# Kernel tuning notes

Hardware: AMD Instinct MI355X
Metric: run time of the kernel (lower is better)

## Reference

```python
import jax, jax.numpy as jnp
import numpy as np

EMBED = 128
HEADS = 4
WS = (7, 7)
N = WS[0] * WS[1]  # 49 patches per window
B_ = 8192          # batch * num_windows_total
NW = 64            # windows per image (for mask reshape)


def _rel_pos_index():
    # Deterministic relative-position index table, computed exactly as in build().
    coords = np.stack(np.meshgrid(np.arange(WS[0]), np.arange(WS[1]), indexing='ij'))
    coords = coords.reshape(2, -1)                     # [2, N]
    rel = coords[:, :, None] - coords[:, None, :]      # [2, N, N]
    rel = rel.transpose(1, 2, 0).astype(np.int64)      # [N, N, 2]
    rel[:, :, 0] += WS[0] - 1
    rel[:, :, 1] += WS[1] - 1
    rel[:, :, 0] *= 2 * WS[1] - 1
    return jnp.asarray(rel.sum(-1))                    # [N, N]

REL_IDX = _rel_pos_index()


def setup_inputs() -> dict:
    key = jax.random.key(0)
    ks = jax.random.split(key, 7)
    return {
        'x': jax.random.normal(ks[0], (B_, N, EMBED), jnp.float32),
        'mask': jax.random.normal(ks[1], (NW, N, N), jnp.float32),
        'qkv_w': jax.random.normal(ks[2], (EMBED, 3 * EMBED), jnp.float32) * 0.02,
        'qkv_b': jax.random.normal(ks[3], (3 * EMBED,), jnp.float32) * 0.02,
        'proj_w': jax.random.normal(ks[4], (EMBED, EMBED), jnp.float32) * 0.02,
        'proj_b': jax.random.normal(ks[5], (EMBED,), jnp.float32) * 0.02,
        'rel_pos_table': jax.random.normal(ks[6], ((2 * WS[0] - 1) * (2 * WS[1] - 1), HEADS), jnp.float32) * 0.02,
    }


def reference(x, mask, qkv_w, qkv_b, proj_w, proj_b, rel_pos_table):
    B, n, C = x.shape
    hd = C // HEADS
    scale = hd ** -0.5
    # qkv projection then faithful row-major reshape [B,N,3C] -> [3,B,H,N,hd]
    qkv = x @ qkv_w + qkv_b                          # [B, N, 3C]
    qkv = qkv.reshape(3, B, HEADS, n, hd)
    q, k, v = qkv[0] * scale, qkv[1], qkv[2]
    attn = jnp.einsum('bhqd,bhkd->bhqk', q, k)       # [B, H, N, N]
    # gathered relative position bias: [N*N, H] -> [H, N, N]
    bias = rel_pos_table[REL_IDX.reshape(-1)].reshape(n, n, HEADS)
    attn = attn + jnp.transpose(bias, (2, 0, 1))[None]
    # additive window mask: reshape to [B/NW, NW, H, N, N]
    attn = attn.reshape(-1, NW, HEADS, n, n) + mask[None, :, None]
    attn = attn.reshape(-1, HEADS, n, n)
    attn = jax.nn.softmax(attn, axis=-1)
    out = jnp.einsum('bhqk,bhkd->bhqd', attn, v)     # [B, H, N, hd]
    out = jnp.transpose(out, (0, 2, 1, 3)).reshape(B, n, C)
    return out @ proj_w + proj_b
```

## Files before the change

### kernel.cpp

```cpp
#include <hip/hip_runtime.h>

typedef __attribute__((ext_vector_type(8))) short short8;
typedef __attribute__((ext_vector_type(4))) float f32x4;

#define Q3 51380224
#define NROWS 401408

#define XB_OFF 0
#define XB_ST 136
#define Q_OFF 8704
#define QK_H 2560
#define QK_ST 40
#define K_OFF 18944
#define VT_OFF 29184
#define VT_H 2304
#define VT_ST 72
#define P_OFF 8704
#define P_ST 72
#define AOUT_OFF 0
#define LDS_EL 38400

#define WQ_EL 0
#define PW_EL 49152
#define T_BYTE 131072

__device__ __forceinline__ unsigned short f2bf(float f) {
    unsigned int u = __float_as_uint(f);
    u += 0x7FFFu + ((u >> 16) & 1u);
    return (unsigned short)(u >> 16);
}

__global__ __launch_bounds__(256) void prep_weights(
    const float* __restrict__ qkv_w, const float* __restrict__ proj_w,
    unsigned short* __restrict__ wq, unsigned short* __restrict__ pw)
{
    int t = blockIdx.x * 256 + threadIdx.x;
    if (t < 49152) {
        int c = t >> 7, k = t & 127;
        wq[t] = f2bf(qkv_w[k * 384 + c]);
    }
    int t2 = t - 49152;
    if (t2 >= 0 && t2 < 16384) {
        int c = t2 >> 7, k = t2 & 127;
        pw[t2] = f2bf(proj_w[k * 128 + c]);
    }
}

__global__ __launch_bounds__(256) void prep_table(
    const float* __restrict__ mask, const float* __restrict__ rpt,
    float* __restrict__ T)
{
    int t = blockIdx.x * 256 + threadIdx.x;
    if (t >= 64 * 4 * 64 * 64) return;
    int j = t & 63, i = (t >> 6) & 63, h = (t >> 12) & 3, w = t >> 14;
    float v;
    if (j >= 49) v = -1e30f;
    else if (i >= 49) v = 0.f;
    else {
        int ri = i / 7, ci = i - ri * 7, rj = j / 7, cj = j - rj * 7;
        int idx = (ri - rj + 6) * 13 + (ci - cj + 6);
        v = (rpt[idx * 4 + h] + mask[(w * 49 + i) * 49 + j]) * 1.4426950408889634f;
    }
    T[t] = v;
}

__global__ __launch_bounds__(512, 4) void winattn(
    const float* __restrict__ x,
    const unsigned short* __restrict__ wq, const unsigned short* __restrict__ pw,
    const float* __restrict__ T,
    const float* __restrict__ qkv_b, const float* __restrict__ proj_b,
    float* __restrict__ out)
{
    __shared__ unsigned short lds[LDS_EL];
    unsigned int* ldsw = (unsigned int*)lds;
    const int b = blockIdx.x;
    const int tid = threadIdx.x;
    const int wid = tid >> 6;
    const int lane = tid & 63;
    const int l15 = lane & 15;
    const int lq = lane >> 4;
    const f32x4 zero = {0.f, 0.f, 0.f, 0.f};
    const float qscale = 0.17677669529663687f * 1.4426950408889634f;

    const int base0 = b * 6272;
    const int r0_0 = base0 / 384,      off_0 = base0 - r0_0 * 384;
    const int base1 = Q3 + base0;
    const int r0_1 = base1 / 384,      off_1 = base1 - r0_1 * 384;
    const int base2 = 2 * Q3 + base0;
    const int r0_2 = base2 / 384,      off_2 = base2 - r0_2 * 384;

    for (int t = tid; t < 4608; t += 512) ldsw[VT_OFF / 2 + t] = 0u;
    for (int t = tid; t < 2400; t += 512) {
        int run = t / 300, rem = t - run * 300;
        int h = run & 3, reg = run >> 2;
        ldsw[(Q_OFF + reg * 10240 + h * QK_H + 49 * QK_ST) / 2 + rem] = 0u;
    }

    for (int t = tid; t < 51 * 32; t += 512) {
        int row = t >> 5, kq = (t & 31) * 4;
        int run = row >= 34 ? 2 : (row >= 17 ? 1 : 0);
        int r0s = run == 2 ? r0_2 : (run == 1 ? r0_1 : r0_0);
        int gr = r0s + row - run * 17;
        float4 v = *(const float4*)&x[gr * 128 + kq];
        uint2 d;
        d.x = (unsigned int)f2bf(v.x) | ((unsigned int)f2bf(v.y) << 16);
        d.y = (unsigned int)f2bf(v.z) | ((unsigned int)f2bf(v.w) << 16);
        *(uint2*)&ldsw[(row * XB_ST + kq) / 2] = d;
    }
    __syncthreads();

    for (int ntj = 0; ntj < 3; ++ntj) {
        const int nt = wid + ntj * 8;
        const int C = nt * 16 + l15;
        short8 bf[4];
        const short8* wrow = (const short8*)&wq[C * 128];
#pragma unroll
        for (int ks = 0; ks < 4; ++ks) bf[ks] = wrow[ks * 4 + lq];
        const float biasv = qkv_b[C];
#pragma unroll
        for (int mt = 0; mt < 4; ++mt) {
            f32x4 acc = zero;
#pragma unroll
            for (int ks = 0; ks < 4; ++ks) {
                short8 a = *(const short8*)&lds[(mt * 16 + l15) * XB_ST + ks * 32 + lq * 8];
                acc = __builtin_amdgcn_mfma_f32_16x16x32_bf16(a, bf[ks], acc, 0, 0, 0);
            }
#pragma unroll
            for (int r = 0; r < 4; ++r) {
                int R = mt * 16 + lq * 4 + r;
                int run = R >= 34 ? 2 : (R >= 17 ? 1 : 0);
                int offs = run == 2 ? off_2 : (run == 1 ? off_1 : off_0);
                int t2 = (R - run * 17) * 384 + C - offs;
                if (t2 >= 0 && t2 < 6272) {
                    int h = t2 / 1568;
                    int rem = t2 - h * 1568;
                    int n = rem >> 5, d = rem & 31;
                    float o = acc[r] + biasv;
                    if (run == 0) o *= qscale;
                    unsigned short val = f2bf(o);
                    if (run == 2) lds[VT_OFF + h * VT_H + d * VT_ST + n] = val;
                    else lds[(run == 1 ? K_OFF : Q_OFF) + h * QK_H + n * QK_ST + d] = val;
                }
            }
        }
    }
    __syncthreads();

    const int h = wid >> 1;
    {
        const int ihalf = wid & 1;
        short8 kf[4];
#pragma unroll
        for (int jt = 0; jt < 4; ++jt)
            kf[jt] = *(const short8*)&lds[K_OFF + h * QK_H + (jt * 16 + l15) * QK_ST + lq * 8];
        f32x4 acc[2][4];
#pragma unroll
        for (int it = 0; it < 2; ++it) {
            short8 qf = *(const short8*)&lds[Q_OFF + h * QK_H + (ihalf * 32 + it * 16 + l15) * QK_ST + lq * 8];
#pragma unroll
            for (int jt = 0; jt < 4; ++jt)
                acc[it][jt] = __builtin_amdgcn_mfma_f32_16x16x32_bf16(qf, kf[jt], zero, 0, 0, 0);
        }
        __syncthreads();
        const float* Tb = T + (((b & 63) * 4 + h) << 12);
#pragma unroll
        for (int it = 0; it < 2; ++it)
#pragma unroll
        for (int r = 0; r < 4; ++r) {
            int i = ihalf * 32 + it * 16 + lq * 4 + r;
            const float* Trow = Tb + i * 64 + l15;
            float s0 = acc[it][0][r] + Trow[0];
            float s1 = acc[it][1][r] + Trow[16];
            float s2 = acc[it][2][r] + Trow[32];
            float s3 = acc[it][3][r] + Trow[48];
            float m = fmaxf(fmaxf(s0, s1), fmaxf(s2, s3));
            m = fmaxf(m, __shfl_xor(m, 1));
            m = fmaxf(m, __shfl_xor(m, 2));
            m = fmaxf(m, __shfl_xor(m, 4));
            m = fmaxf(m, __shfl_xor(m, 8));
            float e0 = exp2f(s0 - m), e1 = exp2f(s1 - m);
            float e2 = exp2f(s2 - m), e3 = exp2f(s3 - m);
            float sum = e0 + e1 + e2 + e3;
            sum += __shfl_xor(sum, 1);
            sum += __shfl_xor(sum, 2);
            sum += __shfl_xor(sum, 4);
            sum += __shfl_xor(sum, 8);
            float inv = 1.f / sum;
            int pb = P_OFF + (h * 64 + i) * P_ST + l15;
            lds[pb +  0] = f2bf(e0 * inv);
            lds[pb + 16] = f2bf(e1 * inv);
            lds[pb + 32] = f2bf(e2 * inv);
            lds[pb + 48] = f2bf(e3 * inv);
        }
    }
    __syncthreads();

    {
        const int dt = wid & 1;
        const int vbase = VT_OFF + h * VT_H + (dt * 16 + l15) * VT_ST + lq * 8;
        short8 vf0 = *(const short8*)&lds[vbase];
        short8 vf1 = *(const short8*)&lds[vbase + 32];
#pragma unroll
        for (int mt = 0; mt < 4; ++mt) {
            int pbase = P_OFF + (h * 64 + mt * 16 + l15) * P_ST + lq * 8;
            short8 a0 = *(const short8*)&lds[pbase];
            short8 a1 = *(const short8*)&lds[pbase + 32];
            f32x4 acc = __builtin_amdgcn_mfma_f32_16x16x32_bf16(a0, vf0, zero, 0, 0, 0);
            acc = __builtin_amdgcn_mfma_f32_16x16x32_bf16(a1, vf1, acc, 0, 0, 0);
#pragma unroll
            for (int r = 0; r < 4; ++r) {
                int i = mt * 16 + lq * 4 + r;
                if (i < 49)
                    lds[AOUT_OFF + i * XB_ST + h * 32 + dt * 16 + l15] = f2bf(acc[r]);
            }
        }
    }
    const int Cp = wid * 16 + l15;
    short8 pf[4];
#pragma unroll
    for (int ks = 0; ks < 4; ++ks)
        pf[ks] = *(const short8*)&pw[Cp * 128 + ks * 32 + lq * 8];
    const float pbv = proj_b[Cp];
    __syncthreads();

#pragma unroll
    for (int mt = 0; mt < 4; ++mt) {
        f32x4 acc = zero;
#pragma unroll
        for (int ks = 0; ks < 4; ++ks) {
            short8 a = *(const short8*)&lds[AOUT_OFF + (mt * 16 + l15) * XB_ST + ks * 32 + lq * 8];
            acc = __builtin_amdgcn_mfma_f32_16x16x32_bf16(a, pf[ks], acc, 0, 0, 0);
        }
#pragma unroll
        for (int r = 0; r < 4; ++r) {
            int R = mt * 16 + lq * 4 + r;
            if (R < 49)
                out[(b * 49 + R) * 128 + Cp] = acc[r] + pbv;
        }
    }
}

extern "C" void kernel_launch(void* const* d_in, const int* in_sizes, int n_in,
                              void* d_out, int out_size, void* d_ws, size_t ws_size,
                              hipStream_t stream) {
    const float* x      = (const float*)d_in[0];
    const float* mask   = (const float*)d_in[1];
    const float* qkv_w  = (const float*)d_in[2];
    const float* qkv_b  = (const float*)d_in[3];
    const float* proj_w = (const float*)d_in[4];
    const float* proj_b = (const float*)d_in[5];
    const float* rpt    = (const float*)d_in[6];
    float* out = (float*)d_out;

    unsigned short* wq = (unsigned short*)d_ws;
    unsigned short* pw = wq + PW_EL - PW_EL + 49152;
    float* T = (float*)((char*)d_ws + T_BYTE);

    prep_weights<<<256, 256, 0, stream>>>(qkv_w, proj_w, wq, pw);
    prep_table<<<4096, 256, 0, stream>>>(mask, rpt, T);
    winattn<<<8192, 512, 0, stream>>>(x, wq, pw, T, qkv_b, proj_b, out);
}
```

Baseline: 307.2 us.

## Precompute QKV scatter-address table and merge prep kernels into one launch

The per-element index arithmetic for scattering QKV results into LDS (division, run selection, bounds checks) is replaced by a precomputed table of LDS addresses. The table is indexed by b%3, since the scatter pattern repeats every three windows, and invalid entries point to a trash slot. The q scale is folded into the x rows converted for the Q run and into the bias, and the two prep kernels are merged into one launch. The aim is to cut integer ALU work and divergence in the QKV epilogue. The cost is an extra global table load per tile and a small added LDS pad.

```diff
diff --git a/kernel.cpp b/kernel.cpp
--- a/kernel.cpp
+++ b/kernel.cpp
@@ -4,7 +4,6 @@
 typedef __attribute__((ext_vector_type(4))) float f32x4;
 
 #define Q3 51380224
-#define NROWS 401408
 
 #define XB_OFF 0
 #define XB_ST 136
@@ -15,14 +14,11 @@
 #define VT_OFF 29184
 #define VT_H 2304
 #define VT_ST 72
+#define TRASH 38400
+#define LDS_EL 38408
 #define P_OFF 8704
 #define P_ST 72
 #define AOUT_OFF 0
-#define LDS_EL 38400
-
-#define WQ_EL 0
-#define PW_EL 49152
-#define T_BYTE 131072
 
 __device__ __forceinline__ unsigned short f2bf(float f) {
     unsigned int u = __float_as_uint(f);
@@ -30,44 +26,65 @@
     return (unsigned short)(u >> 16);
 }
 
-__global__ __launch_bounds__(256) void prep_weights(
+__global__ __launch_bounds__(256) void prep(
     const float* __restrict__ qkv_w, const float* __restrict__ proj_w,
-    unsigned short* __restrict__ wq, unsigned short* __restrict__ pw)
+    const float* __restrict__ mask, const float* __restrict__ rpt,
+    unsigned short* __restrict__ wq, unsigned short* __restrict__ pw,
+    unsigned short* __restrict__ stab, float* __restrict__ T)
 {
     int t = blockIdx.x * 256 + threadIdx.x;
     if (t < 49152) {
         int c = t >> 7, k = t & 127;
         wq[t] = f2bf(qkv_w[k * 384 + c]);
-    }
-    int t2 = t - 49152;
-    if (t2 >= 0 && t2 < 16384) {
-        int c = t2 >> 7, k = t2 & 127;
-        pw[t2] = f2bf(proj_w[k * 128 + c]);
-    }
-}
-
-__global__ __launch_bounds__(256) void prep_table(
-    const float* __restrict__ mask, const float* __restrict__ rpt,
-    float* __restrict__ T)
-{
-    int t = blockIdx.x * 256 + threadIdx.x;
-    if (t >= 64 * 4 * 64 * 64) return;
-    int j = t & 63, i = (t >> 6) & 63, h = (t >> 12) & 3, w = t >> 14;
-    float v;
-    if (j >= 49) v = -1e30f;
-    else if (i >= 49) v = 0.f;
-    else {
-        int ri = i / 7, ci = i - ri * 7, rj = j / 7, cj = j - rj * 7;
-        int idx = (ri - rj + 6) * 13 + (ci - cj + 6);
-        v = (rpt[idx * 4 + h] + mask[(w * 49 + i) * 49 + j]) * 1.4426950408889634f;
-    }
-    T[t] = v;
+        return;
+    }
+    t -= 49152;
+    if (t < 16384) {
+        int c = t >> 7, k = t & 127;
+        pw[t] = f2bf(proj_w[k * 128 + c]);
+        return;
+    }
+    t -= 16384;
+    if (t < 73728) {
+        int R = t & 63;
+        int b3 = t / (384 * 64);
+        int C = (t - b3 * 384 * 64) >> 6;
+        unsigned short el = TRASH;
+        if (R <= 50) {
+            int run = R >= 34 ? 2 : (R >= 17 ? 1 : 0);
+            int sh = run == 0 ? b3 : (run == 1 ? b3 + 2 : b3 + 1);
+            int offs = 128 * (sh % 3);
+            int t2 = (R - run * 17) * 384 + C - offs;
+            if (t2 >= 0 && t2 < 6272) {
+                int h = t2 / 1568;
+                int rem = t2 - h * 1568;
+                int n = rem >> 5, d = rem & 31;
+                el = (run == 2) ? (unsigned short)(VT_OFF + h * VT_H + d * VT_ST + n)
+                   : (unsigned short)((run == 1 ? K_OFF : Q_OFF) + h * QK_H + n * QK_ST + d);
+            }
+        }
+        stab[t] = el;
+        return;
+    }
+    t -= 73728;
+    if (t < 64 * 4 * 64 * 64) {
+        int j = t & 63, i = (t >> 6) & 63, h = (t >> 12) & 3, w = t >> 14;
+        float v;
+        if (j >= 49) v = -1e30f;
+        else if (i >= 49) v = 0.f;
+        else {
+            int ri = i / 7, ci = i - ri * 7, rj = j / 7, cj = j - rj * 7;
+            int idx = (ri - rj + 6) * 13 + (ci - cj + 6);
+            v = (rpt[idx * 4 + h] + mask[(w * 49 + i) * 49 + j]) * 1.4426950408889634f;
+        }
+        T[t] = v;
+    }
 }
 
 __global__ __launch_bounds__(512, 4) void winattn(
     const float* __restrict__ x,
     const unsigned short* __restrict__ wq, const unsigned short* __restrict__ pw,
-    const float* __restrict__ T,
+    const unsigned short* __restrict__ stab, const float* __restrict__ T,
     const float* __restrict__ qkv_b, const float* __restrict__ proj_b,
     float* __restrict__ out)
 {
@@ -81,19 +98,18 @@
     const int lq = lane >> 4;
     const f32x4 zero = {0.f, 0.f, 0.f, 0.f};
     const float qscale = 0.17677669529663687f * 1.4426950408889634f;
+    const int b3 = b % 3;
 
     const int base0 = b * 6272;
-    const int r0_0 = base0 / 384,      off_0 = base0 - r0_0 * 384;
-    const int base1 = Q3 + base0;
-    const int r0_1 = base1 / 384,      off_1 = base1 - r0_1 * 384;
-    const int base2 = 2 * Q3 + base0;
-    const int r0_2 = base2 / 384,      off_2 = base2 - r0_2 * 384;
-
-    for (int t = tid; t < 4608; t += 512) ldsw[VT_OFF / 2 + t] = 0u;
+    const int r0_0 = base0 / 384;
+    const int r0_1 = (Q3 + base0) / 384;
+    const int r0_2 = (2 * Q3 + base0) / 384;
+
+    for (int t = tid; t < 4608; t += 512) ldsw[(VT_OFF >> 1) + t] = 0u;
     for (int t = tid; t < 2400; t += 512) {
         int run = t / 300, rem = t - run * 300;
         int h = run & 3, reg = run >> 2;
-        ldsw[(Q_OFF + reg * 10240 + h * QK_H + 49 * QK_ST) / 2 + rem] = 0u;
+        ldsw[((Q_OFF + reg * 10240 + h * QK_H + 49 * QK_ST) >> 1) + rem] = 0u;
     }
 
     for (int t = tid; t < 51 * 32; t += 512) {
@@ -102,21 +118,24 @@
         int r0s = run == 2 ? r0_2 : (run == 1 ? r0_1 : r0_0);
         int gr = r0s + row - run * 17;
         float4 v = *(const float4*)&x[gr * 128 + kq];
+        float sc = (row < 17) ? qscale : 1.f;
         uint2 d;
-        d.x = (unsigned int)f2bf(v.x) | ((unsigned int)f2bf(v.y) << 16);
-        d.y = (unsigned int)f2bf(v.z) | ((unsigned int)f2bf(v.w) << 16);
-        *(uint2*)&ldsw[(row * XB_ST + kq) / 2] = d;
-    }
-    __syncthreads();
-
+        d.x = (unsigned int)f2bf(v.x * sc) | ((unsigned int)f2bf(v.y * sc) << 16);
+        d.y = (unsigned int)f2bf(v.z * sc) | ((unsigned int)f2bf(v.w * sc) << 16);
+        *(uint2*)&ldsw[(row * XB_ST + kq) >> 1] = d;
+    }
+    __syncthreads();
+
+    const unsigned short* stB = &stab[b3 * 384 * 64];
     for (int ntj = 0; ntj < 3; ++ntj) {
-        const int nt = wid + ntj * 8;
-        const int C = nt * 16 + l15;
+        const int C = (wid + ntj * 8) * 16 + l15;
         short8 bf[4];
         const short8* wrow = (const short8*)&wq[C * 128];
 #pragma unroll
         for (int ks = 0; ks < 4; ++ks) bf[ks] = wrow[ks * 4 + lq];
-        const float biasv = qkv_b[C];
+        const float b1 = qkv_b[C];
+        const float bq = b1 * qscale;
+        const ushort4* stRow = (const ushort4*)&stB[C * 64];
 #pragma unroll
         for (int mt = 0; mt < 4; ++mt) {
             f32x4 acc = zero;
@@ -125,23 +144,12 @@
                 short8 a = *(const short8*)&lds[(mt * 16 + l15) * XB_ST + ks * 32 + lq * 8];
                 acc = __builtin_amdgcn_mfma_f32_16x16x32_bf16(a, bf[ks], acc, 0, 0, 0);
             }
-#pragma unroll
-            for (int r = 0; r < 4; ++r) {
-                int R = mt * 16 + lq * 4 + r;
-                int run = R >= 34 ? 2 : (R >= 17 ? 1 : 0);
-                int offs = run == 2 ? off_2 : (run == 1 ? off_1 : off_0);
-                int t2 = (R - run * 17) * 384 + C - offs;
-                if (t2 >= 0 && t2 < 6272) {
-                    int h = t2 / 1568;
-                    int rem = t2 - h * 1568;
-                    int n = rem >> 5, d = rem & 31;
-                    float o = acc[r] + biasv;
-                    if (run == 0) o *= qscale;
-                    unsigned short val = f2bf(o);
-                    if (run == 2) lds[VT_OFF + h * VT_H + d * VT_ST + n] = val;
-                    else lds[(run == 1 ? K_OFF : Q_OFF) + h * QK_H + n * QK_ST + d] = val;
-                }
-            }
+            ushort4 e = stRow[mt * 4 + lq];
+            int Rb = mt * 16 + lq * 4;
+            lds[e.x] = f2bf(acc[0] + (Rb + 0 < 17 ? bq : b1));
+            lds[e.y] = f2bf(acc[1] + (Rb + 1 < 17 ? bq : b1));
+            lds[e.z] = f2bf(acc[2] + (Rb + 2 < 17 ? bq : b1));
+            lds[e.w] = f2bf(acc[3] + (Rb + 3 < 17 ? bq : b1));
         }
     }
     __syncthreads();
@@ -207,12 +215,12 @@
             short8 a1 = *(const short8*)&lds[pbase + 32];
             f32x4 acc = __builtin_amdgcn_mfma_f32_16x16x32_bf16(a0, vf0, zero, 0, 0, 0);
             acc = __builtin_amdgcn_mfma_f32_16x16x32_bf16(a1, vf1, acc, 0, 0, 0);
-#pragma unroll
-            for (int r = 0; r < 4; ++r) {
-                int i = mt * 16 + lq * 4 + r;
-                if (i < 49)
-                    lds[AOUT_OFF + i * XB_ST + h * 32 + dt * 16 + l15] = f2bf(acc[r]);
-            }
+            int i0 = mt * 16 + lq * 4;
+            int abase = AOUT_OFF + h * 32 + dt * 16 + l15;
+            if (i0 + 0 < 49) lds[abase + (i0 + 0) * XB_ST] = f2bf(acc[0]);
+            if (i0 + 1 < 49) lds[abase + (i0 + 1) * XB_ST] = f2bf(acc[1]);
+            if (i0 + 2 < 49) lds[abase + (i0 + 2) * XB_ST] = f2bf(acc[2]);
+            if (i0 + 3 < 49) lds[abase + (i0 + 3) * XB_ST] = f2bf(acc[3]);
         }
     }
     const int Cp = wid * 16 + l15;
@@ -252,11 +260,11 @@
     const float* rpt    = (const float*)d_in[6];
     float* out = (float*)d_out;
 
-    unsigned short* wq = (unsigned short*)d_ws;
-    unsigned short* pw = wq + PW_EL - PW_EL + 49152;
-    float* T = (float*)((char*)d_ws + T_BYTE);
-
-    prep_weights<<<256, 256, 0, stream>>>(qkv_w, proj_w, wq, pw);
-    prep_table<<<4096, 256, 0, stream>>>(mask, rpt, T);
-    winattn<<<8192, 512, 0, stream>>>(x, wq, pw, T, qkv_b, proj_b, out);
-}
+    unsigned short* wq   = (unsigned short*)d_ws;
+    unsigned short* pw   = (unsigned short*)((char*)d_ws + 98304);
+    unsigned short* stab = (unsigned short*)((char*)d_ws + 131072);
+    float*          T    = (float*)((char*)d_ws + 278528);
+
+    prep<<<4640, 256, 0, stream>>>(qkv_w, proj_w, mask, rpt, wq, pw, stab, T);
+    winattn<<<8192, 512, 0, stream>>>(x, wq, pw, stab, T, qkv_b, proj_b, out);
+}
```

After: 318.8 us. +3.8%, slower.
